# Kernel optimization log

Hardware: AMD Instinct MI355X
Metric: run time of the kernel (lower is better)

## Reference

```python
import jax, jax.numpy as jnp
import numpy as np

B, T, V, H, C = 128, 4096, 128, 256, 10
EPS = 0.1  # args._epsilon (training mode)

def setup_inputs() -> dict:
    key = jax.random.key(0)
    ks = jax.random.split(key, 8)
    rn = lambda k, shape, sc: (jax.random.normal(k, shape, jnp.float32) * sc)
    return {
        "X": rn(ks[0], (B, T, V), 1.0),
        "u": jax.random.uniform(ks[1], (B, T, 1), jnp.float32),
        "Wk": rn(ks[2], (V, 4 * H), 0.05),
        "Wr": rn(ks[3], (H, 4 * H), 0.05),
        "b_lstm": jnp.zeros((4 * H,), jnp.float32),
        "Wo": rn(ks[4], (H, C), 0.05),
        "bo": jnp.zeros((C,), jnp.float32),
        "Wc": rn(ks[5], (H + 1, 1), 0.05),
        "bc": jnp.zeros((1,), jnp.float32),
        "Wb": rn(ks[6], (H + 1, 1), 0.05),
        "bb": jnp.zeros((1,), jnp.float32),
    }

def reference(X, u, Wk, Wr, b_lstm, Wo, bo, Wc, bc, Wb, bb):
    Bn = X.shape[0]
    xT = jnp.swapaxes(X, 0, 1)  # [T,B,V]
    uT = jnp.swapaxes(u, 0, 1)  # [T,B,1]
    ts = jnp.arange(T, dtype=jnp.float32)

    def step(carry, inp):
        h, c, preds, halt = carry
        x_t, u_t, t = inp
        # Keras LSTMCell: gates order i, f, g(c), o
        z = x_t @ Wk + h @ Wr + b_lstm  # [B,4H]
        i, f, g, o = jnp.split(z, 4, axis=1)
        i = jax.nn.sigmoid(i); f = jax.nn.sigmoid(f)
        g = jnp.tanh(g); o = jax.nn.sigmoid(o)
        c = f * c + i * g
        h = o * jnp.tanh(c)
        logits = jax.nn.softmax(h @ Wo + bo, axis=-1)  # softmax Dense
        time = jnp.ones((Bn, 1), jnp.float32) * t
        c_in = jax.lax.stop_gradient(jnp.concatenate([h, time], axis=1))
        p = jax.nn.sigmoid(c_in @ Wc + bc)
        probs = (1.0 - EPS) * p + EPS * 0.05
        a = (u_t < probs).astype(jnp.float32)  # Bernoulli sample via uniform noise
        _b = c_in @ Wb + bb  # baseline (does not affect returned logits)
        preds = jnp.where((a == 1.0) & (preds == 0.0), logits, preds)
        halt = jnp.where((halt == -1.0) & (a == 1.0), time, halt)
        return (h, c, preds, halt), logits

    init = (jnp.zeros((Bn, H), jnp.float32),
            jnp.zeros((Bn, H), jnp.float32),
            jnp.zeros((Bn, C), jnp.float32),
            -jnp.ones((Bn, 1), jnp.float32))
    (h, c, preds, halt), all_logits = jax.lax.scan(step, init, (xT, uT, ts))
    logits_last = all_logits[-1]
    # samples that never halted get the final-step logits
    return jnp.where(preds == 0.0, logits_last, preds)
```

## Files before the change

kernel.cpp:

```cpp
#include <hip/hip_runtime.h>
#include <cstddef>
#include <cstdint>

#define NT_ 4096
#define NV_ 128
#define NH_ 256
#define NC_ 10
#define KT_ 384
#define NGRP 16
#define SB   8
#define GWG  16
#define TPW  256
#define VST  12
#define Z9   9
#define FULLMASK 255

#define SM_W    0
#define SM_V    24576
#define SM_ZP   (SM_V + KT_*VST)
#define SM_C    (SM_ZP + 2304)
#define SM_BL   (SM_C + 144)
#define SM_WC   (SM_BL + 64)
#define SM_WO   (SM_WC + 260)
#define SM_HD   (SM_WO + 2560)
#define SM_RED  (SM_HD + 12)
#define SM_TOT  (SM_RED + 32)
#define SMEM_BYTES (SM_TOT * 4)

#define WS_HBUF  4096

#define ALD(p)    __hip_atomic_load((p), __ATOMIC_RELAXED, __HIP_MEMORY_SCOPE_AGENT)
#define AST(p,v)  __hip_atomic_store((p), (v), __ATOMIC_RELAXED, __HIP_MEMORY_SCOPE_AGENT)

#define FMA8(S) \
  acc[S].x = fmaf(w4.x, vs, acc[S].x); \
  acc[S].y = fmaf(w4.y, vs, acc[S].y); \
  acc[S].z = fmaf(w4.z, vs, acc[S].z); \
  acc[S].w = fmaf(w4.w, vs, acc[S].w);

extern "C" __global__ __launch_bounds__(TPW, 1)
void earliest_coop(const float* __restrict__ X, const float* __restrict__ U,
                   const float* __restrict__ Wk, const float* __restrict__ Wr,
                   const float* __restrict__ bl, const float* __restrict__ Wo,
                   const float* __restrict__ bo, const float* __restrict__ Wc,
                   const float* __restrict__ bc, float* __restrict__ out,
                   int* __restrict__ cnt, float* __restrict__ hbuf)
{
  extern __shared__ float smem[];
  float* w_lds = smem + SM_W;
  float* v_lds = smem + SM_V;
  float* zp    = smem + SM_ZP;
  float* c_lds = smem + SM_C;
  float* bl_s  = smem + SM_BL;
  float* wc_s  = smem + SM_WC;
  float* wo_s  = smem + SM_WO;
  float* hd_s  = smem + SM_HD;
  float* red   = smem + SM_RED;
  __shared__ int halted_lds;
  __shared__ int wflags;

  const int tid  = threadIdx.x;
  const int w    = blockIdx.x & 15;
  const int g    = blockIdx.x >> 4;
  const int colq = tid & 15;
  const int ks   = tid >> 4;
  const bool leader = (w == 0);

  for (int m = 0; m < 24; ++m) {
    int idx4 = m * 256 + tid;
    int k = idx4 >> 4, cq = idx4 & 15;
    int rr = cq >> 2, qq = cq & 3;
    int col4 = rr * 64 + w * 4 + qq;
    float4 wv;
    if (k < NV_) wv = ((const float4*)Wk)[(size_t)k * 256 + col4];
    else         wv = ((const float4*)Wr)[(size_t)(k - NV_) * 256 + col4];
    ((float4*)w_lds)[k * 16 + (cq ^ (k & 7))] = wv;
  }
  if (tid < 64) {
    int rr = tid >> 4, e = tid & 15;
    bl_s[tid] = bl[rr * 256 + w * 16 + e];
  }
  wc_s[tid] = Wc[tid];
  if (tid == 0) wc_s[256] = Wc[256];
  if (tid < 128) c_lds[(tid >> 3) * Z9 + (tid & 7)] = 0.f;
  if (leader) {
    for (int m = tid; m < NH_ * NC_; m += TPW) wo_s[m] = Wo[m];
  }
  if (tid < 10)  hd_s[tid] = bo[tid];
  if (tid == 10) hd_s[10] = bc[0];
  if (tid == 0)  { halted_lds = 0; wflags = 0; }

  int* cntg = cnt + (g << 6);
  const int cswz  = colq ^ (ks & 7);
  const int wbase = ks * 16 + cswz;

  const int xk4 = tid >> 3;
  const int xs  = tid & 7;
  const float4* X4 = (const float4*)X;
  float4 xr = X4[((size_t)(g * SB + xs) * NT_ + 0) * 32 + xk4];

  __syncthreads();
  {
    #pragma unroll
    for (int j = 0; j < 4; ++j)
      v_lds[(4 * xk4 + j) * VST + xs] = ((const float*)&xr)[j];
  }

  float uv_pf = 0.f;

  for (int it = 0;; ++it) {
    if (tid == 0) wflags = 0;
    if (it == 0) {
      #pragma unroll
      for (int i2 = 0; i2 < 8; ++i2) {
        int flat = i2 * 256 + tid;
        v_lds[(NV_ + (flat >> 3)) * VST + (flat & 7)] = 0.f;
      }
    } else {
      const float* hsrc = hbuf + ((size_t)(it & 1) * NGRP + g) * NH_ * SB;
      #pragma unroll
      for (int i2 = 0; i2 < 8; ++i2) {
        int flat = i2 * 256 + tid;
        v_lds[(NV_ + (flat >> 3)) * VST + (flat & 7)] = ALD(hsrc + flat);
      }
    }
    __syncthreads();

    if (it < NT_) {
      if (it + 1 < NT_)
        xr = X4[((size_t)(g * SB + xs) * NT_ + (it + 1)) * 32 + xk4];

      float4 acc[8];
      #pragma unroll
      for (int s = 0; s < 8; ++s) acc[s] = make_float4(0.f, 0.f, 0.f, 0.f);
      {
        const float4* wl4 = (const float4*)w_lds;
        #pragma unroll
        for (int i = 0; i < 24; ++i) {
          int k = i * 16 + ks;
          float4 w4 = wl4[i * 256 + wbase];
          const float* vk = v_lds + k * VST;
          float4 va = *(const float4*)(vk);
          float4 vb = *(const float4*)(vk + 4);
          { float vs = va.x; FMA8(0) } { float vs = va.y; FMA8(1) }
          { float vs = va.z; FMA8(2) } { float vs = va.w; FMA8(3) }
          { float vs = vb.x; FMA8(4) } { float vs = vb.y; FMA8(5) }
          { float vs = vb.z; FMA8(6) } { float vs = vb.w; FMA8(7) }
        }
      }
      #pragma unroll
      for (int off = 16; off <= 32; off <<= 1) {
        #pragma unroll
        for (int s = 0; s < 8; ++s) {
          acc[s].x += __shfl_xor(acc[s].x, off, 64);
          acc[s].y += __shfl_xor(acc[s].y, off, 64);
          acc[s].z += __shfl_xor(acc[s].z, off, 64);
          acc[s].w += __shfl_xor(acc[s].w, off, 64);
        }
      }
      if ((tid & 48) == 0) {
        int w4 = tid >> 6;
        float4* zp4 = (float4*)zp;
        #pragma unroll
        for (int s = 0; s < 8; ++s) zp4[(w4 * 16 + colq) * Z9 + s] = acc[s];
      }
    }
    if (it >= 1) {
      const float* hv = v_lds + (NV_ + tid) * VST;
      const float wcv = wc_s[tid];
      float part[SB];
      #pragma unroll
      for (int s = 0; s < SB; ++s) part[s] = hv[s] * wcv;
      #pragma unroll
      for (int off = 1; off <= 32; off <<= 1) {
        #pragma unroll
        for (int s = 0; s < SB; ++s) part[s] += __shfl_xor(part[s], off, 64);
      }
      if ((tid & 63) == 0) {
        int w4 = tid >> 6;
        #pragma unroll
        for (int s = 0; s < SB; ++s) red[w4 * 8 + s] = part[s];
      }
      if (tid >= 128 && tid < 128 + SB)
        uv_pf = U[(size_t)(g * SB + (tid - 128)) * NT_ + (it - 1)];
    }
    __syncthreads();

    if (it < NT_ && tid < 128) {
      int e = tid >> 3, s = tid & 7;
      float zg4[4];
      #pragma unroll
      for (int r = 0; r < 4; ++r) {
        int cq = r * 4 + (e >> 2);
        int j  = e & 3;
        float sum = 0.f;
        #pragma unroll
        for (int w4 = 0; w4 < 4; ++w4)
          sum += zp[((w4 * 16 + cq) * Z9 + s) * 4 + j];
        zg4[r] = sum + bl_s[r * 16 + e];
      }
      float gi = 1.f / (1.f + expf(-zg4[0]));
      float gf = 1.f / (1.f + expf(-zg4[1]));
      float gg = tanhf(zg4[2]);
      float go = 1.f / (1.f + expf(-zg4[3]));
      float c = gf * c_lds[e * Z9 + s] + gi * gg;
      c_lds[e * Z9 + s] = c;
      float h = go * tanhf(c);
      size_t hidx = (((size_t)((it + 1) & 1) * NGRP + g) * NH_ + (w * 16 + e)) * SB + s;
      AST(hbuf + hidx, h);
    }
    if (it >= 1 && tid >= 128 && tid < 128 + SB) {
      const int s_ = tid - 128;
      if (!((halted_lds >> s_) & 1)) {
        const int tau = it - 1;
        const float psum = red[0 * 8 + s_] + red[1 * 8 + s_] + red[2 * 8 + s_] + red[3 * 8 + s_];
        const float pre   = psum + (float)tau * wc_s[256] + hd_s[10];
        const float p     = 1.f / (1.f + expf(-pre));
        const float probs = 0.9f * p + 0.005f;
        const bool  a     = (uv_pf < probs);
        if (a || tau == NT_ - 1) atomicOr(&wflags, 1 << s_);
        if (a) atomicOr(&halted_lds, 1 << s_);
      }
    }
    __syncthreads();

    if (tid == 0)
      __hip_atomic_fetch_add(cntg, 1, __ATOMIC_RELAXED, __HIP_MEMORY_SCOPE_AGENT);

    if (it + 1 < NT_) {
      #pragma unroll
      for (int j = 0; j < 4; ++j)
        v_lds[(4 * xk4 + j) * VST + xs] = ((const float*)&xr)[j];
    }

    if (it >= 1 && leader && wflags) {
      const int e5 = tid >> 3, s = tid & 7;
      float accv[NC_];
      #pragma unroll
      for (int cc = 0; cc < NC_; ++cc) accv[cc] = 0.f;
      #pragma unroll
      for (int i2 = 0; i2 < 8; ++i2) {
        const int e = i2 * 32 + e5;
        const float hvv = v_lds[(NV_ + e) * VST + s];
        #pragma unroll
        for (int cc = 0; cc < NC_; ++cc) accv[cc] += hvv * wo_s[e * NC_ + cc];
      }
      #pragma unroll
      for (int off = 8; off <= 32; off <<= 1) {
        #pragma unroll
        for (int cc = 0; cc < NC_; ++cc) accv[cc] += __shfl_xor(accv[cc], off, 64);
      }
      if ((tid & 56) == 0) {
        const int w4 = tid >> 6;
        #pragma unroll
        for (int cc = 0; cc < NC_; ++cc) zp[(w4 * 8 + s) * NC_ + cc] = accv[cc];
      }
      __syncthreads();
      if (tid < SB && ((wflags >> tid) & 1)) {
        const int s_ = tid;
        float l[NC_];
        float mx = -1e30f;
        #pragma unroll
        for (int cc = 0; cc < NC_; ++cc) {
          l[cc] = zp[(0 * 8 + s_) * NC_ + cc] + zp[(1 * 8 + s_) * NC_ + cc]
                + zp[(2 * 8 + s_) * NC_ + cc] + zp[(3 * 8 + s_) * NC_ + cc] + hd_s[cc];
          mx = fmaxf(mx, l[cc]);
        }
        float ssum = 0.f;
        #pragma unroll
        for (int cc = 0; cc < NC_; ++cc) { l[cc] = expf(l[cc] - mx); ssum += l[cc]; }
        const float inv = 1.f / ssum;
        float* op = out + (g * SB + s_) * NC_;
        #pragma unroll
        for (int cc = 0; cc < NC_; ++cc) op[cc] = l[cc] * inv;
      }
      __syncthreads();
    }

    if (halted_lds == FULLMASK || it == NT_) break;

    if (tid == 0) {
      const int target = GWG * (it + 1);
      while (ALD(cntg) < target) __builtin_amdgcn_s_sleep(1);
    }
    __syncthreads();
  }
}

extern "C" void kernel_launch(void* const* d_in, const int* in_sizes, int n_in,
                              void* d_out, int out_size, void* d_ws, size_t ws_size,
                              hipStream_t stream)
{
  const float* X  = (const float*)d_in[0];
  const float* U  = (const float*)d_in[1];
  const float* Wk = (const float*)d_in[2];
  const float* Wr = (const float*)d_in[3];
  const float* bL = (const float*)d_in[4];
  const float* Wo = (const float*)d_in[5];
  const float* bo = (const float*)d_in[6];
  const float* Wc = (const float*)d_in[7];
  const float* bc = (const float*)d_in[8];
  float* out = (float*)d_out;

  int*   cnt  = (int*)d_ws;
  float* hbuf = (float*)((char*)d_ws + WS_HBUF);

  hipMemsetAsync(d_ws, 0, WS_HBUF, stream);

  hipFuncSetAttribute((const void*)earliest_coop,
                      hipFuncAttributeMaxDynamicSharedMemorySize, SMEM_BYTES);

  void* args[] = { (void*)&X, (void*)&U, (void*)&Wk, (void*)&Wr, (void*)&bL,
                   (void*)&Wo, (void*)&bo, (void*)&Wc, (void*)&bc, (void*)&out,
                   (void*)&cnt, (void*)&hbuf };
  hipError_t lerr = hipLaunchCooperativeKernel((const void*)earliest_coop,
                                               dim3(NGRP * GWG), dim3(TPW),
                                               args, SMEM_BYTES, stream);
  if (lerr != hipSuccess) {
    hipLaunchKernelGGL(earliest_coop, dim3(NGRP * GWG), dim3(TPW), SMEM_BYTES, stream,
                       X, U, Wk, Wr, bL, Wo, bo, Wc, bc, out, cnt, hbuf);
  }
}
```

Baseline: 183.0 us.

## Precompute input-projection partial sums before the inter-block barrier wait

The first 8 of 24 K-chunks, which cover the X·Wk rows, are accumulated for the next step before the spin-wait on the group counter, so only the 16 recurrent chunks remain after the barrier. This moves input-dependent work off the serial critical path of the recurrence. It also adds an extra __syncthreads per step and, when the workspace is large enough, a nontemporal per-step store into a diagnostic buffer, both of which add overhead.

```diff
diff --git a/kernel.cpp b/kernel.cpp
--- a/kernel.cpp
+++ b/kernel.cpp
@@ -28,6 +28,7 @@
 #define SMEM_BYTES (SM_TOT * 4)
 
 #define WS_HBUF  4096
+#define WS_DIAG  (1u << 20)
 
 #define ALD(p)    __hip_atomic_load((p), __ATOMIC_RELAXED, __HIP_MEMORY_SCOPE_AGENT)
 #define AST(p,v)  __hip_atomic_store((p), (v), __ATOMIC_RELAXED, __HIP_MEMORY_SCOPE_AGENT)
@@ -37,6 +38,18 @@
   acc[S].y = fmaf(w4.y, vs, acc[S].y); \
   acc[S].z = fmaf(w4.z, vs, acc[S].z); \
   acc[S].w = fmaf(w4.w, vs, acc[S].w);
+
+#define ZSTEP(i)                                            \
+  {                                                         \
+    float4 w4 = wl4[(i) * 256 + wbase];                     \
+    const float* vk = v_lds + ((i) * 16 + ks) * VST;        \
+    float4 va = *(const float4*)(vk);                       \
+    float4 vb = *(const float4*)(vk + 4);                   \
+    { float vs = va.x; FMA8(0) } { float vs = va.y; FMA8(1) } \
+    { float vs = va.z; FMA8(2) } { float vs = va.w; FMA8(3) } \
+    { float vs = vb.x; FMA8(4) } { float vs = vb.y; FMA8(5) } \
+    { float vs = vb.z; FMA8(6) } { float vs = vb.w; FMA8(7) } \
+  }
 
 extern "C" __global__ __launch_bounds__(TPW, 1)
 void earliest_coop(const float* __restrict__ X, const float* __restrict__ U,
@@ -44,7 +57,8 @@
                    const float* __restrict__ bl, const float* __restrict__ Wo,
                    const float* __restrict__ bo, const float* __restrict__ Wc,
                    const float* __restrict__ bc, float* __restrict__ out,
-                   int* __restrict__ cnt, float* __restrict__ hbuf)
+                   int* __restrict__ cnt, float* __restrict__ hbuf,
+                   char* __restrict__ diag)
 {
   extern __shared__ float smem[];
   float* w_lds = smem + SM_W;
@@ -93,6 +107,7 @@
   int* cntg = cnt + (g << 6);
   const int cswz  = colq ^ (ks & 7);
   const int wbase = ks * 16 + cswz;
+  const float4* wl4 = (const float4*)w_lds;
 
   const int xk4 = tid >> 3;
   const int xs  = tid & 7;
@@ -105,6 +120,13 @@
     for (int j = 0; j < 4; ++j)
       v_lds[(4 * xk4 + j) * VST + xs] = ((const float*)&xr)[j];
   }
+  __syncthreads();
+
+  float4 acc[8];
+  #pragma unroll
+  for (int s = 0; s < 8; ++s) acc[s] = make_float4(0.f, 0.f, 0.f, 0.f);
+  #pragma unroll
+  for (int i = 0; i < 8; ++i) ZSTEP(i)
 
   float uv_pf = 0.f;
 
@@ -129,25 +151,8 @@
     if (it < NT_) {
       if (it + 1 < NT_)
         xr = X4[((size_t)(g * SB + xs) * NT_ + (it + 1)) * 32 + xk4];
-
-      float4 acc[8];
-      #pragma unroll
-      for (int s = 0; s < 8; ++s) acc[s] = make_float4(0.f, 0.f, 0.f, 0.f);
-      {
-        const float4* wl4 = (const float4*)w_lds;
-        #pragma unroll
-        for (int i = 0; i < 24; ++i) {
-          int k = i * 16 + ks;
-          float4 w4 = wl4[i * 256 + wbase];
-          const float* vk = v_lds + k * VST;
-          float4 va = *(const float4*)(vk);
-          float4 vb = *(const float4*)(vk + 4);
-          { float vs = va.x; FMA8(0) } { float vs = va.y; FMA8(1) }
-          { float vs = va.z; FMA8(2) } { float vs = va.w; FMA8(3) }
-          { float vs = vb.x; FMA8(4) } { float vs = vb.y; FMA8(5) }
-          { float vs = vb.z; FMA8(6) } { float vs = vb.w; FMA8(7) }
-        }
-      }
+      #pragma unroll
+      for (int i = 8; i < 24; ++i) ZSTEP(i)
       #pragma unroll
       for (int off = 16; off <= 32; off <<= 1) {
         #pragma unroll
@@ -224,8 +229,12 @@
     }
     __syncthreads();
 
-    if (tid == 0)
+    if (tid == 0) {
       __hip_atomic_fetch_add(cntg, 1, __ATOMIC_RELAXED, __HIP_MEMORY_SCOPE_AGENT);
+      if (diag)
+        __builtin_nontemporal_store(1u,
+            (uint32_t*)(diag + (((size_t)blockIdx.x << 8) + (it & 255)) * 64));
+    }
 
     if (it + 1 < NT_) {
       #pragma unroll
@@ -278,6 +287,15 @@
     }
 
     if (halted_lds == FULLMASK || it == NT_) break;
+
+    __syncthreads();
+
+    #pragma unroll
+    for (int s = 0; s < 8; ++s) acc[s] = make_float4(0.f, 0.f, 0.f, 0.f);
+    if (it + 1 < NT_) {
+      #pragma unroll
+      for (int i = 0; i < 8; ++i) ZSTEP(i)
+    }
 
     if (tid == 0) {
       const int target = GWG * (it + 1);
@@ -304,6 +322,7 @@
 
   int*   cnt  = (int*)d_ws;
   float* hbuf = (float*)((char*)d_ws + WS_HBUF);
+  char*  diag = (ws_size >= (6u << 20)) ? ((char*)d_ws + WS_DIAG) : nullptr;
 
   hipMemsetAsync(d_ws, 0, WS_HBUF, stream);
 
@@ -312,12 +331,12 @@
 
   void* args[] = { (void*)&X, (void*)&U, (void*)&Wk, (void*)&Wr, (void*)&bL,
                    (void*)&Wo, (void*)&bo, (void*)&Wc, (void*)&bc, (void*)&out,
-                   (void*)&cnt, (void*)&hbuf };
+                   (void*)&cnt, (void*)&hbuf, (void*)&diag };
   hipError_t lerr = hipLaunchCooperativeKernel((const void*)earliest_coop,
                                                dim3(NGRP * GWG), dim3(TPW),
                                                args, SMEM_BYTES, stream);
   if (lerr != hipSuccess) {
     hipLaunchKernelGGL(earliest_coop, dim3(NGRP * GWG), dim3(TPW), SMEM_BYTES, stream,
-                       X, U, Wk, Wr, bL, Wo, bo, Wc, bc, out, cnt, hbuf);
+                       X, U, Wk, Wr, bL, Wo, bo, Wc, bc, out, cnt, hbuf, diag);
   }
 }
```

Measured after the change: 181.4 us. No clear change (-0.9%).
